# Optimization experiments

Measured on AMD Instinct MI355X. Metric: run time of the kernel, lower is better.

Reference implementation:

```python
import jax, jax.numpy as jnp
import numpy as np
from jax import lax


def setup_inputs() -> dict:
    key = jax.random.key(0)
    k1, k2 = jax.random.split(key)
    B, C = 128, 256
    z_f = jax.random.normal(k1, (B, C, 7, 7), dtype=jnp.float32)
    x_f = jax.random.normal(k2, (B, C, 31, 31), dtype=jnp.float32)
    return {"z_f": z_f, "x_f": x_f}


def xcorr_depthwise(search, kernel):
    # search: [B, C, Hx, Wx], kernel: [B, C, Hz, Wz]
    B, C, Hx, Wx = search.shape
    _, _, Hz, Wz = kernel.shape
    s = search.reshape(1, B * C, Hx, Wx)          # [1, B*C, Hx, Wx]
    k = kernel.reshape(B * C, 1, Hz, Wz)          # [B*C, 1, Hz, Wz]
    out = lax.conv_general_dilated(
        s, k,
        window_strides=(1, 1),
        padding='VALID',
        dimension_numbers=('NCHW', 'OIHW', 'NCHW'),
        feature_group_count=B * C,
    )                                             # [1, B*C, Ho, Wo]
    Ho, Wo = Hx - Hz + 1, Wx - Wz + 1
    return out.reshape(B, C, Ho, Wo)


def reference(z_f, x_f):
    # DepthwiseRPN.forward: xcorr_depthwise(search=x_f, kernel=z_f)
    return xcorr_depthwise(x_f, z_f)
```

## Files before the change

kernel.cpp:

```cpp
#include <hip/hip_runtime.h>


#define PPB 10
#define WX 31
#define XPLANE 961
#define ZPLANE 49
#define OPLANE 625
#define WO 25
#define XCHUNKS 38
#define XSLOTS (XCHUNKS * 256)
#define ZCHUNKS 2
#define ZSLOTS (ZCHUNKS * 256)

typedef __attribute__((address_space(1))) const void gaddr_t;
typedef __attribute__((address_space(3))) void laddr_t;

__global__ __launch_bounds__(256) void dwxcorr_kernel(
    const float* __restrict__ z, const float* __restrict__ x,
    float* __restrict__ out, int nplanes) {
  __shared__ float xs[XSLOTS];
  __shared__ float zs[ZSLOTS];

  const int tid = threadIdx.x;
  const int p0 = blockIdx.x * PPB;
  const int pmax = min(PPB, nplanes - p0);
  const long XTOT = (long)nplanes * XPLANE;
  const long ZTOT = (long)nplanes * ZPLANE;
  const long xoff = (long)p0 * XPLANE;
  const long zoff = (long)p0 * ZPLANE;
  const int wbase = tid & ~63;

#pragma unroll
  for (int c = 0; c < XCHUNKS; ++c) {
    long gi = xoff + c * 256 + tid;
    if (gi >= XTOT) gi = XTOT - 1;
    __builtin_amdgcn_global_load_lds((gaddr_t*)(x + gi),
                                     (laddr_t*)&xs[c * 256 + wbase], 4, 0, 0);
  }
#pragma unroll
  for (int c = 0; c < ZCHUNKS; ++c) {
    long gi = zoff + c * 256 + tid;
    if (gi >= ZTOT) gi = ZTOT - 1;
    __builtin_amdgcn_global_load_lds((gaddr_t*)(z + gi),
                                     (laddr_t*)&zs[c * 256 + wbase], 4, 0, 0);
  }
  __syncthreads();

  const int pp = tid / 25;
  if (pp >= pmax) return;
  const int t25 = tid - pp * 25;
  const int ty = t25 / 5;
  const int tx = t25 - ty * 5;

  float zr[ZPLANE];
#pragma unroll
  for (int j = 0; j < ZPLANE; ++j) zr[j] = zs[pp * ZPLANE + j];

  float acc[5][5];
#pragma unroll
  for (int r = 0; r < 5; ++r)
#pragma unroll
    for (int j = 0; j < 5; ++j) acc[r][j] = 0.0f;

  const float* xbase = &xs[pp * XPLANE + (ty * 5) * WX + tx * 5];

#pragma unroll
  for (int iy = 0; iy < 11; ++iy) {
    float xr[11];
#pragma unroll
    for (int k = 0; k < 11; ++k) xr[k] = xbase[iy * WX + k];
    const int ky_lo = (iy - 4 < 0) ? 0 : iy - 4;
    const int ky_hi = (iy < 6) ? iy : 6;
#pragma unroll
    for (int ky = 0; ky < 7; ++ky) {
      if (ky < ky_lo || ky > ky_hi) continue;
      const int orow = iy - ky;
#pragma unroll
      for (int kx = 0; kx < 7; ++kx) {
        const float zv = zr[ky * 7 + kx];
#pragma unroll
        for (int j = 0; j < 5; ++j)
          acc[orow][j] = fmaf(xr[kx + j], zv, acc[orow][j]);
      }
    }
  }

  float* ob = out + (size_t)(p0 + pp) * OPLANE + (ty * 5) * WO + tx * 5;
#pragma unroll
  for (int r = 0; r < 5; ++r)
#pragma unroll
    for (int j = 0; j < 5; ++j) ob[r * WO + j] = acc[r][j];
}

extern "C" void kernel_launch(void* const* d_in, const int* in_sizes, int n_in,
                              void* d_out, int out_size, void* d_ws, size_t ws_size,
                              hipStream_t stream) {
  const float* z = (const float*)d_in[0];
  const float* x = (const float*)d_in[1];
  float* out = (float*)d_out;

  const int nplanes = in_sizes[0] / ZPLANE;
  const int blocks = (nplanes + PPB - 1) / PPB;

  hipLaunchKernelGGL(dwxcorr_kernel, dim3(blocks), dim3(256), 0, stream,
                     z, x, out, nplanes);
}
```

Before: 50.73 us.

## Pad LDS row stride to reduce bank conflicts and use 8 planes per block

Each search plane is now stored in shared memory with a padded row stride of 37 instead of 31, remapping the global-to-LDS load indices so that threads reading neighbouring 5x5 output tiles hit fewer LDS bank conflicts. Planes per block drop from 10 to 8, which also removes the tail bounds checks because 32768 divides evenly by 8. A launch-bounds occupancy hint of 4 blocks is added. The padding costs extra LDS and some wasted duplicate loads, and fewer planes per block means more blocks with a smaller share of active threads (200 of 256).

```diff
diff --git a/kernel.cpp b/kernel.cpp
--- a/kernel.cpp
+++ b/kernel.cpp
@@ -1,21 +1,25 @@
 #include <hip/hip_runtime.h>
 
 
-#define PPB 10
+#define PPB 8
 #define WX 31
+#define RS 37
 #define XPLANE 961
+#define LDSPLANE (31 * RS)
 #define ZPLANE 49
 #define OPLANE 625
 #define WO 25
-#define XCHUNKS 38
+#define XFLOATS (PPB * LDSPLANE)
+#define XCHUNKS ((XFLOATS + 255) / 256)
 #define XSLOTS (XCHUNKS * 256)
+#define ZFLOATS (PPB * ZPLANE)
 #define ZCHUNKS 2
 #define ZSLOTS (ZCHUNKS * 256)
 
 typedef __attribute__((address_space(1))) const void gaddr_t;
 typedef __attribute__((address_space(3))) void laddr_t;
 
-__global__ __launch_bounds__(256) void dwxcorr_kernel(
+__global__ __launch_bounds__(256, 4) void dwxcorr_kernel(
     const float* __restrict__ z, const float* __restrict__ x,
     float* __restrict__ out, int nplanes) {
   __shared__ float xs[XSLOTS];
@@ -23,31 +27,40 @@
 
   const int tid = threadIdx.x;
   const int p0 = blockIdx.x * PPB;
-  const int pmax = min(PPB, nplanes - p0);
-  const long XTOT = (long)nplanes * XPLANE;
-  const long ZTOT = (long)nplanes * ZPLANE;
   const long xoff = (long)p0 * XPLANE;
   const long zoff = (long)p0 * ZPLANE;
   const int wbase = tid & ~63;
 
+  {
+    int slot0 = tid;
+    int pp = 0, rem = tid;
 #pragma unroll
-  for (int c = 0; c < XCHUNKS; ++c) {
-    long gi = xoff + c * 256 + tid;
-    if (gi >= XTOT) gi = XTOT - 1;
-    __builtin_amdgcn_global_load_lds((gaddr_t*)(x + gi),
-                                     (laddr_t*)&xs[c * 256 + wbase], 4, 0, 0);
+    for (int c = 0; c < XCHUNKS; ++c) {
+      int rr = rem;
+      int ppc = pp;
+      if (c == XCHUNKS - 1 && ppc >= PPB) { ppc = PPB - 1; rr = LDSPLANE - 1; }
+      int r = rr / RS;
+      int col = rr - r * RS;
+      col = (col > 30) ? 30 : col;
+      long gi = xoff + ppc * XPLANE + r * WX + col;
+      __builtin_amdgcn_global_load_lds((gaddr_t*)(x + gi),
+                                       (laddr_t*)&xs[c * 256 + wbase], 4, 0, 0);
+      rem += 256;
+      if (rem >= LDSPLANE) { rem -= LDSPLANE; pp++; }
+      (void)slot0;
+    }
   }
 #pragma unroll
   for (int c = 0; c < ZCHUNKS; ++c) {
-    long gi = zoff + c * 256 + tid;
-    if (gi >= ZTOT) gi = ZTOT - 1;
-    __builtin_amdgcn_global_load_lds((gaddr_t*)(z + gi),
+    int s = c * 256 + tid;
+    if (s >= ZFLOATS) s = ZFLOATS - 1;
+    __builtin_amdgcn_global_load_lds((gaddr_t*)(z + zoff + s),
                                      (laddr_t*)&zs[c * 256 + wbase], 4, 0, 0);
   }
   __syncthreads();
 
+  if (tid >= PPB * 25) return;
   const int pp = tid / 25;
-  if (pp >= pmax) return;
   const int t25 = tid - pp * 25;
   const int ty = t25 / 5;
   const int tx = t25 - ty * 5;
@@ -62,13 +75,13 @@
 #pragma unroll
     for (int j = 0; j < 5; ++j) acc[r][j] = 0.0f;
 
-  const float* xbase = &xs[pp * XPLANE + (ty * 5) * WX + tx * 5];
+  const float* xbase = &xs[pp * LDSPLANE + (ty * 5) * RS + tx * 5];
 
 #pragma unroll
   for (int iy = 0; iy < 11; ++iy) {
     float xr[11];
 #pragma unroll
-    for (int k = 0; k < 11; ++k) xr[k] = xbase[iy * WX + k];
+    for (int k = 0; k < 11; ++k) xr[k] = xbase[iy * RS + k];
     const int ky_lo = (iy - 4 < 0) ? 0 : iy - 4;
     const int ky_hi = (iy < 6) ? iy : 6;
 #pragma unroll
```

New measurement: 60.79 us. 1.2x slower.

## Use 5x13 output strips per thread with swizzled padded LDS and 16-byte loads

Applied to the files above, without the earlier changes.

Each thread now computes a 5-row by 13-column output strip instead of a 5x5 tile, raising register reuse of loaded input rows. Blocks shrink to 128 threads and cover 12 planes each. Each plane is stored in LDS with a 32-float row pitch (plane stride 1032) and an XOR swizzle, so compute can use float4 reads without bank conflicts. Full blocks fill LDS with 16-byte global-to-LDS DMA loads, and the tail block keeps a scalar fallback path. The costs are higher register pressure, about 4 of 64 lanes per wave idle, and one block per CU under the launch bounds, which lowers occupancy.

```diff
diff --git a/kernel.cpp b/kernel.cpp
--- a/kernel.cpp
+++ b/kernel.cpp
@@ -1,74 +1,53 @@
 #include <hip/hip_runtime.h>
 
 
-#define PPB 10
+#define PPB 12
 #define WX 31
 #define XPLANE 961
+#define PSTR 1032
+#define XDW (PPB * PSTR)
+#define XALLOC 12800
+#define ZSTR 52
 #define ZPLANE 49
+#define ZDW (PPB * ZSTR)
 #define OPLANE 625
 #define WO 25
-#define XCHUNKS 38
-#define XSLOTS (XCHUNKS * 256)
-#define ZCHUNKS 2
-#define ZSLOTS (ZCHUNKS * 256)
 
 typedef __attribute__((address_space(1))) const void gaddr_t;
 typedef __attribute__((address_space(3))) void laddr_t;
 
-__global__ __launch_bounds__(256) void dwxcorr_kernel(
-    const float* __restrict__ z, const float* __restrict__ x,
-    float* __restrict__ out, int nplanes) {
-  __shared__ float xs[XSLOTS];
-  __shared__ float zs[ZSLOTS];
+template <int S>
+__device__ __forceinline__ void strip_compute(const float* lds, int cpp,
+                                              int ty, long plane, float* out) {
+  const float* zl = lds + XALLOC + cpp * ZSTR;
+  float zr[49];
+#pragma unroll
+  for (int i = 0; i < 12; ++i) {
+    float4 v = *(const float4*)(zl + i * 4);
+    zr[i * 4 + 0] = v.x; zr[i * 4 + 1] = v.y;
+    zr[i * 4 + 2] = v.z; zr[i * 4 + 3] = v.w;
+  }
+  zr[48] = zl[48];
 
-  const int tid = threadIdx.x;
-  const int p0 = blockIdx.x * PPB;
-  const int pmax = min(PPB, nplanes - p0);
-  const long XTOT = (long)nplanes * XPLANE;
-  const long ZTOT = (long)nplanes * ZPLANE;
-  const long xoff = (long)p0 * XPLANE;
-  const long zoff = (long)p0 * ZPLANE;
-  const int wbase = tid & ~63;
-
-#pragma unroll
-  for (int c = 0; c < XCHUNKS; ++c) {
-    long gi = xoff + c * 256 + tid;
-    if (gi >= XTOT) gi = XTOT - 1;
-    __builtin_amdgcn_global_load_lds((gaddr_t*)(x + gi),
-                                     (laddr_t*)&xs[c * 256 + wbase], 4, 0, 0);
-  }
-#pragma unroll
-  for (int c = 0; c < ZCHUNKS; ++c) {
-    long gi = zoff + c * 256 + tid;
-    if (gi >= ZTOT) gi = ZTOT - 1;
-    __builtin_amdgcn_global_load_lds((gaddr_t*)(z + gi),
-                                     (laddr_t*)&zs[c * 256 + wbase], 4, 0, 0);
-  }
-  __syncthreads();
-
-  const int pp = tid / 25;
-  if (pp >= pmax) return;
-  const int t25 = tid - pp * 25;
-  const int ty = t25 / 5;
-  const int tx = t25 - ty * 5;
-
-  float zr[ZPLANE];
-#pragma unroll
-  for (int j = 0; j < ZPLANE; ++j) zr[j] = zs[pp * ZPLANE + j];
-
-  float acc[5][5];
+  float acc[5][13];
 #pragma unroll
   for (int r = 0; r < 5; ++r)
 #pragma unroll
-    for (int j = 0; j < 5; ++j) acc[r][j] = 0.0f;
+    for (int j = 0; j < 13; ++j) acc[r][j] = 0.0f;
 
-  const float* xbase = &xs[pp * XPLANE + (ty * 5) * WX + tx * 5];
-
+  const float* pb = lds + cpp * PSTR;
 #pragma unroll
   for (int iy = 0; iy < 11; ++iy) {
-    float xr[11];
+    const int row = ty * 5 + iy;
+    const int fc = row & 7;
+    const float* rp = pb + (row << 5);
+    float rb_[20];
 #pragma unroll
-    for (int k = 0; k < 11; ++k) xr[k] = xbase[iy * WX + k];
+    for (int u = 0; u < 5; ++u) {
+      float4 v = *(const float4*)(rp + (((3 * S + u) ^ fc) << 2));
+      rb_[u * 4 + 0] = v.x; rb_[u * 4 + 1] = v.y;
+      rb_[u * 4 + 2] = v.z; rb_[u * 4 + 3] = v.w;
+    }
     const int ky_lo = (iy - 4 < 0) ? 0 : iy - 4;
     const int ky_hi = (iy < 6) ? iy : 6;
 #pragma unroll
@@ -79,17 +58,106 @@
       for (int kx = 0; kx < 7; ++kx) {
         const float zv = zr[ky * 7 + kx];
 #pragma unroll
-        for (int j = 0; j < 5; ++j)
-          acc[orow][j] = fmaf(xr[kx + j], zv, acc[orow][j]);
+        for (int j = 0; j < 13; ++j)
+          acc[orow][j] = fmaf(rb_[j + kx + S], zv, acc[orow][j]);
       }
     }
   }
 
-  float* ob = out + (size_t)(p0 + pp) * OPLANE + (ty * 5) * WO + tx * 5;
+  float* ob = out + plane * OPLANE + 13 * S;
 #pragma unroll
-  for (int r = 0; r < 5; ++r)
+  for (int r = 0; r < 5; ++r) {
+    float* orow = ob + (ty * 5 + r) * WO;
 #pragma unroll
-    for (int j = 0; j < 5; ++j) ob[r * WO + j] = acc[r][j];
+    for (int j = 0; j < 13 - S; ++j) orow[j] = acc[r][j];
+  }
+}
+
+__global__ __launch_bounds__(128, 1) void dwxcorr_kernel(
+    const float* __restrict__ z, const float* __restrict__ x,
+    float* __restrict__ out, int nplanes) {
+  __shared__ float lds[XALLOC + ZDW];
+
+  const int tid = threadIdx.x;
+  const int wb4 = (tid & ~63) * 4;
+  const int wb1 = tid & ~63;
+  const int p0 = blockIdx.x * PPB;
+  const int pmax = min(PPB, nplanes - p0);
+  const long XTOT = (long)nplanes * XPLANE;
+  const long ZTOT = (long)nplanes * ZPLANE;
+  const long xoff = (long)p0 * XPLANE;
+  const long zoff = (long)p0 * ZPLANE;
+
+  if (p0 + PPB < nplanes) {
+#pragma unroll
+    for (int it = 0; it < 25; ++it) {
+      int s = it * 512 + tid * 4;
+      unsigned p = (unsigned)s / PSTR;
+      int r = s - (int)p * PSTR;
+      if (p >= PPB) { p = PPB - 1; r = 30 << 5; }
+      int row = r >> 5;
+      int q = r & 31;
+      int qq = q ^ ((row & 7) << 2);
+      long g = xoff + (long)p * XPLANE + row * WX + qq;
+      __builtin_amdgcn_global_load_lds((gaddr_t*)(x + g),
+                                       (laddr_t*)&lds[it * 512 + wb4], 16, 0, 0);
+    }
+#pragma unroll
+    for (int it = 0; it < 2; ++it) {
+      if (it == 0 || tid < 28) {
+        int s = it * 512 + tid * 4;
+        unsigned p = (unsigned)s / ZSTR;
+        int col = s - (int)p * ZSTR;
+        long g = zoff + (long)p * ZPLANE + col;
+        __builtin_amdgcn_global_load_lds((gaddr_t*)(z + g),
+                                         (laddr_t*)&lds[XALLOC + it * 512 + wb4],
+                                         16, 0, 0);
+      }
+    }
+  } else {
+#pragma unroll
+    for (int it = 0; it < 100; ++it) {
+      int s = it * 128 + tid;
+      if (s < XALLOC) {
+        unsigned p = (unsigned)s / PSTR;
+        int r = s - (int)p * PSTR;
+        if ((int)p >= pmax) { p = pmax - 1; r = 30 << 5; }
+        int row = r >> 5;
+        int col = (r & 31) ^ ((row & 7) << 2);
+        long g = xoff + (long)p * XPLANE + row * WX + col;
+        if (g > XTOT - 1) g = XTOT - 1;
+        __builtin_amdgcn_global_load_lds((gaddr_t*)(x + g),
+                                         (laddr_t*)&lds[it * 128 + wb1], 4, 0, 0);
+      }
+    }
+#pragma unroll
+    for (int it = 0; it < 5; ++it) {
+      int s = it * 128 + tid;
+      if (s < ZDW) {
+        unsigned p = (unsigned)s / ZSTR;
+        int col = s - (int)p * ZSTR;
+        if ((int)p >= pmax) p = pmax - 1;
+        col = (col > 48) ? 48 : col;
+        long g = zoff + (long)p * ZPLANE + col;
+        if (g > ZTOT - 1) g = ZTOT - 1;
+        __builtin_amdgcn_global_load_lds((gaddr_t*)(z + g),
+                                         (laddr_t*)&lds[XALLOC + it * 128 + wb1],
+                                         4, 0, 0);
+      }
+    }
+  }
+  __syncthreads();
+
+  const int wave = tid >> 6;
+  const int lane = tid & 63;
+  const int cpp = lane / 5;
+  const int ty = lane - cpp * 5;
+  if (lane >= 60 || cpp >= pmax) return;
+
+  if (wave == 0)
+    strip_compute<0>(lds, cpp, ty, (long)(p0 + cpp), out);
+  else
+    strip_compute<1>(lds, cpp, ty, (long)(p0 + cpp), out);
 }
 
 extern "C" void kernel_launch(void* const* d_in, const int* in_sizes, int n_in,
@@ -102,6 +170,6 @@
   const int nplanes = in_sizes[0] / ZPLANE;
   const int blocks = (nplanes + PPB - 1) / PPB;
 
-  hipLaunchKernelGGL(dwxcorr_kernel, dim3(blocks), dim3(256), 0, stream,
+  hipLaunchKernelGGL(dwxcorr_kernel, dim3(blocks), dim3(128), 0, stream,
                      z, x, out, nplanes);
 }
```

Result: slower. 73.86 us (+45.6%).
